# Kernel tuning notes

Measured on AMD Instinct MI355X. Metric: run time of the kernel, lower is better.

The kernel has to match this reference:

```python
import jax, jax.numpy as jnp
import numpy as np

ALPHA = 0.2  # LeakyReLU slope in GAT
OUT_SLOPE = 0.01  # default nn.LeakyyReLU slope for self.out
B, E, IN_DIM, HID, HEADS = 4, 2048, 32, 18, 3
DH = HID // HEADS  # per-head out dim = 6


def _leaky(x, slope):
    return jnp.where(x > 0, x, slope * x)


def _gat_head(x, adj, W, a):
    # x: [B,E,in], W: [in,dh], a: [2*dh,1]
    h = jnp.einsum('bei,id->bed', x, W)                      # [B,E,dh]
    d = h.shape[-1]
    # score[b,i,j] = leakyrelu(a . concat(h_i, h_j)) = leakyrelu(h_i.a1 + h_j.a2)
    e1 = jnp.einsum('bed,d->be', h, a[:d, 0])
    e2 = jnp.einsum('bed,d->be', h, a[d:, 0])
    score = _leaky(e1[:, :, None] + e2[:, None, :], ALPHA)   # [B,E,E]
    scores = jnp.where(adj == 1.0, score, 0.0)
    logits = jnp.where(adj > 0.0, scores, -30.0)
    att = jax.nn.softmax(logits, axis=2)                     # softmax over j
    # h_prime[b,j,d] = sum_i att[b,i,j] * h[b,i,d]  (torch sums over dim=1)
    h_prime = jnp.einsum('bij,bid->bjd', att, h)
    return jax.nn.elu(h_prime)  # concat=True -> elu


def _gat_multihead(x, adj, Ws, As):
    # Ws: [H,in,dh], As: [H,2*dh,1]
    outs = jax.vmap(lambda W, a: _gat_head(x, adj, W, a))(Ws, As)  # [H,B,E,dh]
    H, b, e, d = outs.shape
    return jnp.moveaxis(outs, 0, 2).reshape(b, e, H * d)  # concat heads last-dim


def _gcn(x, adj2d, W, b):
    return adj2d @ (x @ W) + b


def setup_inputs() -> dict:
    key = jax.random.key(0)
    ks = jax.random.split(key, 16)
    node_input = jax.random.normal(ks[0], (B, E, IN_DIM), jnp.float32)
    uv_filed = jax.random.normal(ks[1], (B, E, IN_DIM), jnp.float32)
    adj = jax.random.randint(ks[2], (B, E, E), 0, 2).astype(jnp.float32)
    s = 0.1
    Wt1 = jax.random.normal(ks[3], (HEADS, IN_DIM, DH), jnp.float32) * s
    at1 = jax.random.normal(ks[4], (HEADS, 2 * DH, 1), jnp.float32) * s
    Wt2 = jax.random.normal(ks[5], (HEADS, IN_DIM, DH), jnp.float32) * s
    at2 = jax.random.normal(ks[6], (HEADS, 2 * DH, 1), jnp.float32) * s
    Wg1 = jax.random.normal(ks[7], (HID, 16), jnp.float32) * s
    bg1 = jnp.zeros((16,), jnp.float32)
    Wg2 = jax.random.normal(ks[8], (16, 2), jnp.float32) * s
    bg2 = jnp.zeros((2,), jnp.float32)
    Wo1 = jax.random.normal(ks[9], (HID, 16), jnp.float32) * s
    bo1 = jnp.zeros((16,), jnp.float32)
    Wo2 = jax.random.normal(ks[10], (16, 2), jnp.float32) * s
    bo2 = jnp.zeros((2,), jnp.float32)
    return dict(node_input=node_input, uv_filed=uv_filed, adj=adj,
                Wt1=Wt1, at1=at1, Wt2=Wt2, at2=at2,
                Wg1=Wg1, bg1=bg1, Wg2=Wg2, bg2=bg2,
                Wo1=Wo1, bo1=bo1, Wo2=Wo2, bo2=bo2)


def reference(node_input, uv_filed, adj, Wt1, at1, Wt2, at2,
              Wg1, bg1, Wg2, bg2, Wo1, bo1, Wo2, bo2):
    h = _gat_multihead(node_input, adj, Wt1, at1)  # [B,E,18]
    o = _gat_multihead(uv_filed, adj, Wt2, at2)    # [B,E,18]
    a0 = adj[0]
    Y = jax.nn.relu(_gcn(h[0], a0, Wg1, bg1))
    O = jax.nn.relu(_gcn(o[0], a0, Wo1, bo1))
    Y = _gcn(Y, a0, Wg2, bg2)
    O = _gcn(O, a0, Wo2, bo2)
    return (jax.nn.log_softmax(Y, axis=1), _leaky(O, OUT_SLOPE))
```

## Files before the change

kernel.cpp:

```cpp
#include <hip/hip_runtime.h>
#include <hip/hip_bf16.h>


__global__ __launch_bounds__(256) void k1_features(
    const float* __restrict__ node, const float* __restrict__ uv,
    const float* __restrict__ Wt1, const float* __restrict__ at1,
    const float* __restrict__ Wt2, const float* __restrict__ at2,
    float* __restrict__ hcol, float* __restrict__ pack1, float* __restrict__ pack2) {
  __shared__ float sW[192];
  __shared__ float sA[12];
  int b = blockIdx.x;
  int g = b / 24;
  int h = (b / 8) % 3;
  int e = (b % 8) * 256 + threadIdx.x;
  const float* W = (g ? Wt2 : Wt1) + h * 192;
  const float* A = (g ? at2 : at1) + h * 12;
  const float* x = (g ? uv : node) + e * 32;
  if (threadIdx.x < 192) sW[threadIdx.x] = W[threadIdx.x];
  if (threadIdx.x < 12) sA[threadIdx.x] = A[threadIdx.x];
  __syncthreads();
  float xv[32];
#pragma unroll
  for (int i = 0; i < 32; ++i) xv[i] = x[i];
  float hv[6];
#pragma unroll
  for (int d = 0; d < 6; ++d) hv[d] = 0.f;
#pragma unroll
  for (int i = 0; i < 32; ++i)
#pragma unroll
    for (int d = 0; d < 6; ++d) hv[d] += xv[i] * sW[i * 6 + d];
  float e1 = 0.f, e2 = 0.f;
#pragma unroll
  for (int d = 0; d < 6; ++d) {
    e1 += hv[d] * sA[d];
    e2 += hv[d] * sA[6 + d];
  }
  int c = g * 3 + h;
#pragma unroll
  for (int d = 0; d < 6; ++d) hcol[(c * 6 + d) * 2048 + e] = hv[d];
  pack1[c * 2048 + e] = e1;
  pack1[(6 + c) * 2048 + e] = __expf(e1);
  pack1[(12 + c) * 2048 + e] = __expf(0.2f * e1);
  pack2[c * 2048 + e] = e2;
  pack2[(6 + c) * 2048 + e] = __expf(e2);
  pack2[(12 + c) * 2048 + e] = __expf(0.2f * e2);
}

__global__ __launch_bounds__(384) void k2_rowsum(
    const float* __restrict__ adj0, const float* __restrict__ pack1,
    const float* __restrict__ pack2, float* __restrict__ invrs) {
  int tid = threadIdx.x;
  int c = tid >> 6, lane = tid & 63;
  int i0 = blockIdx.x * 4;
  const float4* adj4 = (const float4*)adj0;
  const float4* p2_4 = (const float4*)pack2;
  float e1r[4], p1r[4], q1r[4], sum[4];
#pragma unroll
  for (int r = 0; r < 4; ++r) {
    e1r[r] = pack1[c * 2048 + i0 + r];
    p1r[r] = pack1[(6 + c) * 2048 + i0 + r];
    q1r[r] = pack1[(12 + c) * 2048 + i0 + r];
    sum[r] = 0.f;
  }
#pragma unroll
  for (int it = 0; it < 8; ++it) {
    int j4 = it * 64 + lane;
    float4 e2 = p2_4[c * 512 + j4];
    float4 p2 = p2_4[(6 + c) * 512 + j4];
    float4 q2 = p2_4[(12 + c) * 512 + j4];
    float4 av[4];
#pragma unroll
    for (int r = 0; r < 4; ++r) av[r] = adj4[(i0 + r) * 512 + j4];
#pragma unroll
    for (int r = 0; r < 4; ++r) {
      float s0, s1, s2, s3;
      { float e = e1r[r] + e2.x; bool p = e > 0.f;
        s0 = av[r].x * (p ? p1r[r] : q1r[r]) * (p ? p2.x : q2.x); }
      { float e = e1r[r] + e2.y; bool p = e > 0.f;
        s1 = av[r].y * (p ? p1r[r] : q1r[r]) * (p ? p2.y : q2.y); }
      { float e = e1r[r] + e2.z; bool p = e > 0.f;
        s2 = av[r].z * (p ? p1r[r] : q1r[r]) * (p ? p2.z : q2.z); }
      { float e = e1r[r] + e2.w; bool p = e > 0.f;
        s3 = av[r].w * (p ? p1r[r] : q1r[r]) * (p ? p2.w : q2.w); }
      sum[r] += (s0 + s1) + (s2 + s3);
    }
  }
#pragma unroll
  for (int r = 0; r < 4; ++r) {
#pragma unroll
    for (int off = 32; off > 0; off >>= 1) sum[r] += __shfl_down(sum[r], off);
  }
  if (lane == 0) {
#pragma unroll
    for (int r = 0; r < 4; ++r) invrs[c * 2048 + i0 + r] = 1.0f / sum[r];
  }
}

__global__ __launch_bounds__(384) void k3_hprime(
    const float* __restrict__ adj0, const float* __restrict__ hcol,
    const float* __restrict__ pack1, const float* __restrict__ pack2,
    const float* __restrict__ invrs, float* __restrict__ hp) {
  __shared__ float sAdj[64 * 64];
  __shared__ float4 sPack[6 * 64];
  __shared__ float sHS[6 * 64 * 8];
  float4* sAdj4 = (float4*)sAdj;
  const float4* adj4 = (const float4*)adj0;
  float4* sHS4 = (float4*)sHS;
  int tid = threadIdx.x;
  int c6 = tid >> 6, jl = tid & 63;
  int j0 = blockIdx.x * 64;
  int j = j0 + jl;
  float e2v = pack2[c6 * 2048 + j];
  float p2v = pack2[(6 + c6) * 2048 + j];
  float q2v = pack2[(12 + c6) * 2048 + j];
  float acc0 = 0.f, acc1 = 0.f, acc2 = 0.f, acc3 = 0.f, acc4 = 0.f, acc5 = 0.f;
  int ibeg = blockIdx.y * 128, iend = ibeg + 128;
  for (int i0 = ibeg; i0 < iend; i0 += 64) {
    __syncthreads();
    for (int idx = tid; idx < 1024; idx += 384) {
      int ii = idx >> 4, c4 = idx & 15;
      sAdj4[ii * 16 + c4] = adj4[(i0 + ii) * 512 + (j0 >> 2) + c4];
    }
    {
      int cc = c6, ii = jl;
      float e1 = pack1[cc * 2048 + i0 + ii];
      float p1 = pack1[(6 + cc) * 2048 + i0 + ii];
      float q1 = pack1[(12 + cc) * 2048 + i0 + ii];
      sPack[cc * 64 + ii] = make_float4(e1, p1, q1, 0.f);
      float iv = invrs[cc * 2048 + i0 + ii];
#pragma unroll
      for (int d = 0; d < 6; ++d)
        sHS[(cc * 64 + ii) * 8 + d] = hcol[(cc * 6 + d) * 2048 + i0 + ii] * iv;
      sHS[(cc * 64 + ii) * 8 + 6] = 0.f;
      sHS[(cc * 64 + ii) * 8 + 7] = 0.f;
    }
    __syncthreads();
#pragma unroll 8
    for (int ii = 0; ii < 64; ++ii) {
      float adjv = sAdj[ii * 64 + jl];
      float4 pk = sPack[c6 * 64 + ii];
      float4 h0 = sHS4[(c6 * 64 + ii) * 2];
      float4 h1 = sHS4[(c6 * 64 + ii) * 2 + 1];
      float e = pk.x + e2v;
      bool pos = e > 0.f;
      float w = adjv * (pos ? pk.y : pk.z) * (pos ? p2v : q2v);
      acc0 += w * h0.x;
      acc1 += w * h0.y;
      acc2 += w * h0.z;
      acc3 += w * h0.w;
      acc4 += w * h1.x;
      acc5 += w * h1.y;
    }
  }
  int kb = c6 * 6;
  atomicAdd(&hp[(kb + 0) * 2048 + j], acc0);
  atomicAdd(&hp[(kb + 1) * 2048 + j], acc1);
  atomicAdd(&hp[(kb + 2) * 2048 + j], acc2);
  atomicAdd(&hp[(kb + 3) * 2048 + j], acc3);
  atomicAdd(&hp[(kb + 4) * 2048 + j], acc4);
  atomicAdd(&hp[(kb + 5) * 2048 + j], acc5);
}

__global__ __launch_bounds__(256) void k4_T(
    const float* __restrict__ hp, const float* __restrict__ Wg1,
    const float* __restrict__ Wo1, float* __restrict__ T) {
  __shared__ float sHP[32 * 37];
  __shared__ float sWg[288], sWo[288];
  int tid = threadIdx.x;
  int j0 = blockIdx.x * 32;
  for (int idx = tid; idx < 288; idx += 256) {
    sWg[idx] = Wg1[idx];
    sWo[idx] = Wo1[idx];
  }
  for (int idx = tid; idx < 1152; idx += 256) {
    int r = idx >> 5, jl = idx & 31;
    sHP[jl * 37 + r] = hp[r * 2048 + j0 + jl];
  }
  __syncthreads();
  int jl = tid & 31, wq = tid >> 5;
  int gat = wq >> 2;
  int c0 = (wq & 3) * 4;
  const float* Wp = gat ? sWo : sWg;
  float acc[4];
#pragma unroll
  for (int t = 0; t < 4; ++t) acc[t] = 0.f;
#pragma unroll
  for (int r = 0; r < 18; ++r) {
    float x = sHP[jl * 37 + gat * 18 + r];
    float hc = x > 0.f ? x : __expf(x) - 1.f;
#pragma unroll
    for (int t = 0; t < 4; ++t) acc[t] += hc * Wp[r * 16 + c0 + t];
  }
#pragma unroll
  for (int t = 0; t < 4; ++t) T[(j0 + jl) * 32 + gat * 16 + c0 + t] = acc[t];
}

__global__ __launch_bounds__(256) void k5_gcn1(
    const float* __restrict__ adj0, const float* __restrict__ T,
    float* __restrict__ Craw) {
  int tid = threadIdx.x;
  int lane = tid & 63, w = tid >> 6;
  int c = lane & 31, rh = lane >> 5;
  int r = blockIdx.x * 8 + w * 2 + rh;
  int k0 = blockIdx.y * 512;
  const float* arow = adj0 + (size_t)r * 2048 + k0;
  const float* tcol = T + (size_t)k0 * 32 + c;
  float acc = 0.f;
#pragma unroll 16
  for (int k = 0; k < 512; ++k) {
    acc += arow[k] * tcol[k * 32];
  }
  atomicAdd(&Craw[r * 32 + c], acc);
}

__global__ __launch_bounds__(256) void k6_T2(
    const float* __restrict__ Craw, const float* __restrict__ bg1,
    const float* __restrict__ Wg2, const float* __restrict__ bo1,
    const float* __restrict__ Wo2, float* __restrict__ T2) {
  int tid = threadIdx.x;
  int wave = tid >> 6, lane = tid & 63;
  int j = blockIdx.x * 8 + wave * 2 + (lane >> 5);
  int cl = lane & 31;
  int gat = cl >> 4, cc = cl & 15;
  float x = Craw[j * 32 + cl];
  x += gat ? bo1[cc] : bg1[cc];
  x = x > 0.f ? x : 0.f;
  float wa = gat ? Wo2[cc * 2 + 0] : Wg2[cc * 2 + 0];
  float wb = gat ? Wo2[cc * 2 + 1] : Wg2[cc * 2 + 1];
  float pa = x * wa, pb = x * wb;
#pragma unroll
  for (int m = 8; m > 0; m >>= 1) {
    pa += __shfl_xor(pa, m);
    pb += __shfl_xor(pb, m);
  }
  if (cc == 0) {
    T2[j * 4 + gat * 2 + 0] = pa;
    T2[j * 4 + gat * 2 + 1] = pb;
  }
}

__global__ __launch_bounds__(256) void k7_final(
    const float* __restrict__ adj0, const float* __restrict__ T2,
    const float* __restrict__ bg2, const float* __restrict__ bo2,
    float* __restrict__ out) {
  int tid = threadIdx.x;
  int lane = tid & 63, w = tid >> 6;
  int r = blockIdx.x * 4 + w;
  const float4* adj4 = (const float4*)adj0;
  const float4* T24 = (const float4*)T2;
  float4 acc = make_float4(0.f, 0.f, 0.f, 0.f);
#pragma unroll
  for (int it = 0; it < 8; ++it) {
    int k4 = it * 64 + lane;
    float4 av = adj4[r * 512 + k4];
    float4 t0 = T24[k4 * 4 + 0];
    float4 t1 = T24[k4 * 4 + 1];
    float4 t2 = T24[k4 * 4 + 2];
    float4 t3 = T24[k4 * 4 + 3];
    acc.x += av.x * t0.x + av.y * t1.x + av.z * t2.x + av.w * t3.x;
    acc.y += av.x * t0.y + av.y * t1.y + av.z * t2.y + av.w * t3.y;
    acc.z += av.x * t0.z + av.y * t1.z + av.z * t2.z + av.w * t3.z;
    acc.w += av.x * t0.w + av.y * t1.w + av.z * t2.w + av.w * t3.w;
  }
#pragma unroll
  for (int off = 32; off > 0; off >>= 1) {
    acc.x += __shfl_down(acc.x, off);
    acc.y += __shfl_down(acc.y, off);
    acc.z += __shfl_down(acc.z, off);
    acc.w += __shfl_down(acc.w, off);
  }
  if (lane == 0) {
    float y0 = acc.x + bg2[0], y1 = acc.y + bg2[1];
    float m = fmaxf(y0, y1);
    float ls = m + logf(__expf(y0 - m) + __expf(y1 - m));
    out[r * 2 + 0] = y0 - ls;
    out[r * 2 + 1] = y1 - ls;
    float o0 = acc.z + bo2[0], o1 = acc.w + bo2[1];
    out[4096 + r * 2 + 0] = o0 > 0.f ? o0 : 0.01f * o0;
    out[4096 + r * 2 + 1] = o1 > 0.f ? o1 : 0.01f * o1;
  }
}

extern "C" void kernel_launch(void* const* d_in, const int* in_sizes, int n_in,
                              void* d_out, int out_size, void* d_ws, size_t ws_size,
                              hipStream_t stream) {
  const float* node = (const float*)d_in[0];
  const float* uv = (const float*)d_in[1];
  const float* adj = (const float*)d_in[2];
  const float* Wt1 = (const float*)d_in[3];
  const float* at1 = (const float*)d_in[4];
  const float* Wt2 = (const float*)d_in[5];
  const float* at2 = (const float*)d_in[6];
  const float* Wg1 = (const float*)d_in[7];
  const float* bg1 = (const float*)d_in[8];
  const float* Wg2 = (const float*)d_in[9];
  const float* bg2 = (const float*)d_in[10];
  const float* Wo1 = (const float*)d_in[11];
  const float* bo1 = (const float*)d_in[12];
  const float* Wo2 = (const float*)d_in[13];
  const float* bo2 = (const float*)d_in[14];
  float* ws = (float*)d_ws;
  float* hcol = ws;
  float* pack1 = ws + 73728;
  float* pack2 = ws + 110592;
  float* invrs = ws + 147456;
  float* T = ws + 159744;
  float* T2 = ws + 225280;
  float* hp = ws + 233472;
  float* Craw = ws + 307200;
  float* out = (float*)d_out;

  hipMemsetAsync(hp, 0, (73728 + 65536) * sizeof(float), stream);
  k1_features<<<48, 256, 0, stream>>>(node, uv, Wt1, at1, Wt2, at2, hcol, pack1, pack2);
  k2_rowsum<<<512, 384, 0, stream>>>(adj, pack1, pack2, invrs);
  k3_hprime<<<dim3(32, 16), 384, 0, stream>>>(adj, hcol, pack1, pack2, invrs, hp);
  k4_T<<<64, 256, 0, stream>>>(hp, Wg1, Wo1, T);
  k5_gcn1<<<dim3(256, 4), 256, 0, stream>>>(adj, T, Craw);
  k6_T2<<<256, 256, 0, stream>>>(Craw, bg1, Wg2, bo1, Wo2, T2);
  k7_final<<<512, 256, 0, stream>>>(adj, T2, bg2, bo2, out);
}
```

Baseline: 196.6 us.

## Compress adjacency into a bitmask once and read it in all adj-consuming kernels

A new first kernel packs the 2048x2048 float adjacency row into 32-bit ballot masks. The rowsum, h-prime aggregation, and both GCN matmul kernels then read bits instead of the 16MB float matrix. The h-prime and GCN-1 kernels are also retiled: h-prime gets 128-column tiles with two accumulator sets per thread and no inner i-loop, and GCN-1 stages the mask and T tiles in shared memory. This cuts repeated global reads of adj, at the cost of an extra launch. It assumes adjacency entries are exactly 0 or 1.

```diff
diff --git a/kernel.cpp b/kernel.cpp
--- a/kernel.cpp
+++ b/kernel.cpp
@@ -1,6 +1,20 @@
 #include <hip/hip_runtime.h>
 #include <hip/hip_bf16.h>
 
+
+__global__ __launch_bounds__(256) void k0_bitmask(
+    const float* __restrict__ adj0, unsigned int* __restrict__ bm) {
+  int lane = threadIdx.x & 63, w = threadIdx.x >> 6;
+  int row = blockIdx.x * 4 + w;
+  const float* arow = adj0 + (size_t)row * 2048;
+#pragma unroll 4
+  for (int it = 0; it < 32; ++it) {
+    float v = arow[it * 64 + lane];
+    unsigned long long mask = __ballot(v == 1.0f);
+    if (lane == 0) bm[row * 64 + it * 2] = (unsigned int)mask;
+    else if (lane == 32) bm[row * 64 + it * 2 + 1] = (unsigned int)(mask >> 32);
+  }
+}
 
 __global__ __launch_bounds__(256) void k1_features(
     const float* __restrict__ node, const float* __restrict__ uv,
@@ -47,118 +61,129 @@
 }
 
 __global__ __launch_bounds__(384) void k2_rowsum(
-    const float* __restrict__ adj0, const float* __restrict__ pack1,
+    const unsigned int* __restrict__ bm, const float* __restrict__ pack1,
     const float* __restrict__ pack2, float* __restrict__ invrs) {
   int tid = threadIdx.x;
   int c = tid >> 6, lane = tid & 63;
-  int i0 = blockIdx.x * 4;
-  const float4* adj4 = (const float4*)adj0;
+  int i0 = blockIdx.x * 8;
   const float4* p2_4 = (const float4*)pack2;
-  float e1r[4], p1r[4], q1r[4], sum[4];
-#pragma unroll
-  for (int r = 0; r < 4; ++r) {
+  float e1r[8], p1r[8], q1r[8], sum[8];
+#pragma unroll
+  for (int r = 0; r < 8; ++r) {
     e1r[r] = pack1[c * 2048 + i0 + r];
     p1r[r] = pack1[(6 + c) * 2048 + i0 + r];
     q1r[r] = pack1[(12 + c) * 2048 + i0 + r];
     sum[r] = 0.f;
   }
+  int sh = (lane & 7) * 4;
 #pragma unroll
   for (int it = 0; it < 8; ++it) {
     int j4 = it * 64 + lane;
     float4 e2 = p2_4[c * 512 + j4];
     float4 p2 = p2_4[(6 + c) * 512 + j4];
     float4 q2 = p2_4[(12 + c) * 512 + j4];
-    float4 av[4];
-#pragma unroll
-    for (int r = 0; r < 4; ++r) av[r] = adj4[(i0 + r) * 512 + j4];
-#pragma unroll
-    for (int r = 0; r < 4; ++r) {
-      float s0, s1, s2, s3;
+    int wbase = it * 8 + (lane >> 3);
+    float abx, aby, abz, abw;
+#pragma unroll
+    for (int r = 0; r < 8; ++r) {
+      unsigned int wd = bm[(i0 + r) * 64 + wbase] >> sh;
       { float e = e1r[r] + e2.x; bool p = e > 0.f;
-        s0 = av[r].x * (p ? p1r[r] : q1r[r]) * (p ? p2.x : q2.x); }
+        abx = (p ? p1r[r] : q1r[r]) * (p ? p2.x : q2.x); }
       { float e = e1r[r] + e2.y; bool p = e > 0.f;
-        s1 = av[r].y * (p ? p1r[r] : q1r[r]) * (p ? p2.y : q2.y); }
+        aby = (p ? p1r[r] : q1r[r]) * (p ? p2.y : q2.y); }
       { float e = e1r[r] + e2.z; bool p = e > 0.f;
-        s2 = av[r].z * (p ? p1r[r] : q1r[r]) * (p ? p2.z : q2.z); }
+        abz = (p ? p1r[r] : q1r[r]) * (p ? p2.z : q2.z); }
       { float e = e1r[r] + e2.w; bool p = e > 0.f;
-        s3 = av[r].w * (p ? p1r[r] : q1r[r]) * (p ? p2.w : q2.w); }
-      sum[r] += (s0 + s1) + (s2 + s3);
+        abw = (p ? p1r[r] : q1r[r]) * (p ? p2.w : q2.w); }
+      float s = ((wd & 1u) ? abx : 0.f) + ((wd & 2u) ? aby : 0.f) +
+                ((wd & 4u) ? abz : 0.f) + ((wd & 8u) ? abw : 0.f);
+      sum[r] += s;
     }
   }
 #pragma unroll
-  for (int r = 0; r < 4; ++r) {
+  for (int r = 0; r < 8; ++r) {
 #pragma unroll
     for (int off = 32; off > 0; off >>= 1) sum[r] += __shfl_down(sum[r], off);
   }
   if (lane == 0) {
 #pragma unroll
-    for (int r = 0; r < 4; ++r) invrs[c * 2048 + i0 + r] = 1.0f / sum[r];
+    for (int r = 0; r < 8; ++r) invrs[c * 2048 + i0 + r] = 1.0f / sum[r];
   }
 }
 
 __global__ __launch_bounds__(384) void k3_hprime(
-    const float* __restrict__ adj0, const float* __restrict__ hcol,
+    const unsigned int* __restrict__ bm, const float* __restrict__ hcol,
     const float* __restrict__ pack1, const float* __restrict__ pack2,
     const float* __restrict__ invrs, float* __restrict__ hp) {
-  __shared__ float sAdj[64 * 64];
   __shared__ float4 sPack[6 * 64];
   __shared__ float sHS[6 * 64 * 8];
-  float4* sAdj4 = (float4*)sAdj;
-  const float4* adj4 = (const float4*)adj0;
+  __shared__ unsigned int sM[64 * 4];
   float4* sHS4 = (float4*)sHS;
   int tid = threadIdx.x;
   int c6 = tid >> 6, jl = tid & 63;
-  int j0 = blockIdx.x * 64;
-  int j = j0 + jl;
-  float e2v = pack2[c6 * 2048 + j];
-  float p2v = pack2[(6 + c6) * 2048 + j];
-  float q2v = pack2[(12 + c6) * 2048 + j];
-  float acc0 = 0.f, acc1 = 0.f, acc2 = 0.f, acc3 = 0.f, acc4 = 0.f, acc5 = 0.f;
-  int ibeg = blockIdx.y * 128, iend = ibeg + 128;
-  for (int i0 = ibeg; i0 < iend; i0 += 64) {
-    __syncthreads();
-    for (int idx = tid; idx < 1024; idx += 384) {
-      int ii = idx >> 4, c4 = idx & 15;
-      sAdj4[ii * 16 + c4] = adj4[(i0 + ii) * 512 + (j0 >> 2) + c4];
+  int j0 = blockIdx.x * 128;
+  int i0 = blockIdx.y * 64;
+  int jA = j0 + jl, jB = jA + 64;
+  float e2A = pack2[c6 * 2048 + jA];
+  float p2A = pack2[(6 + c6) * 2048 + jA];
+  float q2A = pack2[(12 + c6) * 2048 + jA];
+  float e2B = pack2[c6 * 2048 + jB];
+  float p2B = pack2[(6 + c6) * 2048 + jB];
+  float q2B = pack2[(12 + c6) * 2048 + jB];
+  {
+    int cc = c6, ii = jl;
+    float e1 = pack1[cc * 2048 + i0 + ii];
+    float p1 = pack1[(6 + cc) * 2048 + i0 + ii];
+    float q1 = pack1[(12 + cc) * 2048 + i0 + ii];
+    sPack[cc * 64 + ii] = make_float4(e1, p1, q1, 0.f);
+    float iv = invrs[cc * 2048 + i0 + ii];
+#pragma unroll
+    for (int d = 0; d < 6; ++d)
+      sHS[(cc * 64 + ii) * 8 + d] = hcol[(cc * 6 + d) * 2048 + i0 + ii] * iv;
+    sHS[(cc * 64 + ii) * 8 + 6] = 0.f;
+    sHS[(cc * 64 + ii) * 8 + 7] = 0.f;
+  }
+  if (tid < 256) sM[tid] = bm[(size_t)(i0 + (tid >> 2)) * 64 + (j0 >> 5) + (tid & 3)];
+  __syncthreads();
+  float aA0 = 0.f, aA1 = 0.f, aA2 = 0.f, aA3 = 0.f, aA4 = 0.f, aA5 = 0.f;
+  float aB0 = 0.f, aB1 = 0.f, aB2 = 0.f, aB3 = 0.f, aB4 = 0.f, aB5 = 0.f;
+  int hi = jl >> 5;
+  int shj = jl & 31;
+#pragma unroll 8
+  for (int ii = 0; ii < 64; ++ii) {
+    float4 pk = sPack[c6 * 64 + ii];
+    float4 h0 = sHS4[(c6 * 64 + ii) * 2];
+    float4 h1 = sHS4[(c6 * 64 + ii) * 2 + 1];
+    unsigned int wdA = sM[ii * 4 + hi];
+    unsigned int wdB = sM[ii * 4 + 2 + hi];
+    {
+      float e = pk.x + e2A; bool p = e > 0.f;
+      float ab = (p ? pk.y : pk.z) * (p ? p2A : q2A);
+      float wgt = ((wdA >> shj) & 1u) ? ab : 0.f;
+      aA0 += wgt * h0.x; aA1 += wgt * h0.y; aA2 += wgt * h0.z;
+      aA3 += wgt * h0.w; aA4 += wgt * h1.x; aA5 += wgt * h1.y;
     }
     {
-      int cc = c6, ii = jl;
-      float e1 = pack1[cc * 2048 + i0 + ii];
-      float p1 = pack1[(6 + cc) * 2048 + i0 + ii];
-      float q1 = pack1[(12 + cc) * 2048 + i0 + ii];
-      sPack[cc * 64 + ii] = make_float4(e1, p1, q1, 0.f);
-      float iv = invrs[cc * 2048 + i0 + ii];
-#pragma unroll
-      for (int d = 0; d < 6; ++d)
-        sHS[(cc * 64 + ii) * 8 + d] = hcol[(cc * 6 + d) * 2048 + i0 + ii] * iv;
-      sHS[(cc * 64 + ii) * 8 + 6] = 0.f;
-      sHS[(cc * 64 + ii) * 8 + 7] = 0.f;
+      float e = pk.x + e2B; bool p = e > 0.f;
+      float ab = (p ? pk.y : pk.z) * (p ? p2B : q2B);
+      float wgt = ((wdB >> shj) & 1u) ? ab : 0.f;
+      aB0 += wgt * h0.x; aB1 += wgt * h0.y; aB2 += wgt * h0.z;
+      aB3 += wgt * h0.w; aB4 += wgt * h1.x; aB5 += wgt * h1.y;
     }
-    __syncthreads();
-#pragma unroll 8
-    for (int ii = 0; ii < 64; ++ii) {
-      float adjv = sAdj[ii * 64 + jl];
-      float4 pk = sPack[c6 * 64 + ii];
-      float4 h0 = sHS4[(c6 * 64 + ii) * 2];
-      float4 h1 = sHS4[(c6 * 64 + ii) * 2 + 1];
-      float e = pk.x + e2v;
-      bool pos = e > 0.f;
-      float w = adjv * (pos ? pk.y : pk.z) * (pos ? p2v : q2v);
-      acc0 += w * h0.x;
-      acc1 += w * h0.y;
-      acc2 += w * h0.z;
-      acc3 += w * h0.w;
-      acc4 += w * h1.x;
-      acc5 += w * h1.y;
-    }
   }
   int kb = c6 * 6;
-  atomicAdd(&hp[(kb + 0) * 2048 + j], acc0);
-  atomicAdd(&hp[(kb + 1) * 2048 + j], acc1);
-  atomicAdd(&hp[(kb + 2) * 2048 + j], acc2);
-  atomicAdd(&hp[(kb + 3) * 2048 + j], acc3);
-  atomicAdd(&hp[(kb + 4) * 2048 + j], acc4);
-  atomicAdd(&hp[(kb + 5) * 2048 + j], acc5);
+  atomicAdd(&hp[(kb + 0) * 2048 + jA], aA0);
+  atomicAdd(&hp[(kb + 1) * 2048 + jA], aA1);
+  atomicAdd(&hp[(kb + 2) * 2048 + jA], aA2);
+  atomicAdd(&hp[(kb + 3) * 2048 + jA], aA3);
+  atomicAdd(&hp[(kb + 4) * 2048 + jA], aA4);
+  atomicAdd(&hp[(kb + 5) * 2048 + jA], aA5);
+  atomicAdd(&hp[(kb + 0) * 2048 + jB], aB0);
+  atomicAdd(&hp[(kb + 1) * 2048 + jB], aB1);
+  atomicAdd(&hp[(kb + 2) * 2048 + jB], aB2);
+  atomicAdd(&hp[(kb + 3) * 2048 + jB], aB3);
+  atomicAdd(&hp[(kb + 4) * 2048 + jB], aB4);
+  atomicAdd(&hp[(kb + 5) * 2048 + jB], aB5);
 }
 
 __global__ __launch_bounds__(256) void k4_T(
@@ -196,21 +221,39 @@
 }
 
 __global__ __launch_bounds__(256) void k5_gcn1(
-    const float* __restrict__ adj0, const float* __restrict__ T,
+    const unsigned int* __restrict__ bm, const float* __restrict__ T,
     float* __restrict__ Craw) {
-  int tid = threadIdx.x;
-  int lane = tid & 63, w = tid >> 6;
-  int c = lane & 31, rh = lane >> 5;
-  int r = blockIdx.x * 8 + w * 2 + rh;
-  int k0 = blockIdx.y * 512;
-  const float* arow = adj0 + (size_t)r * 2048 + k0;
-  const float* tcol = T + (size_t)k0 * 32 + c;
-  float acc = 0.f;
+  __shared__ unsigned int sM[64 * 4];
+  __shared__ float4 sT4[128 * 8];
+  const float4* T4 = (const float4*)T;
+  int tid = threadIdx.x;
+  int rl = tid & 31, cg = tid >> 5;
+  int i0 = blockIdx.x * 64;
+  int k0 = blockIdx.y * 128;
+  if (tid < 256) sM[tid] = bm[(size_t)(i0 + (tid >> 2)) * 64 + (k0 >> 5) + (tid & 3)];
+  for (int idx = tid; idx < 1024; idx += 256) sT4[idx] = T4[k0 * 8 + idx];
+  __syncthreads();
+  float a0x = 0.f, a0y = 0.f, a0z = 0.f, a0w = 0.f;
+  float a1x = 0.f, a1y = 0.f, a1z = 0.f, a1w = 0.f;
+#pragma unroll
+  for (int wi = 0; wi < 4; ++wi) {
+    unsigned int wA = sM[rl * 4 + wi];
+    unsigned int wB = sM[(rl + 32) * 4 + wi];
 #pragma unroll 16
-  for (int k = 0; k < 512; ++k) {
-    acc += arow[k] * tcol[k * 32];
-  }
-  atomicAdd(&Craw[r * 32 + c], acc);
+    for (int kb = 0; kb < 32; ++kb) {
+      float4 t = sT4[(wi * 32 + kb) * 8 + cg];
+      float mA = (float)((wA >> kb) & 1u);
+      float mB = (float)((wB >> kb) & 1u);
+      a0x += mA * t.x; a0y += mA * t.y; a0z += mA * t.z; a0w += mA * t.w;
+      a1x += mB * t.x; a1y += mB * t.y; a1z += mB * t.z; a1w += mB * t.w;
+    }
+  }
+  float* d0 = &Craw[(i0 + rl) * 32 + cg * 4];
+  atomicAdd(d0 + 0, a0x); atomicAdd(d0 + 1, a0y);
+  atomicAdd(d0 + 2, a0z); atomicAdd(d0 + 3, a0w);
+  float* d1 = &Craw[(i0 + rl + 32) * 32 + cg * 4];
+  atomicAdd(d1 + 0, a1x); atomicAdd(d1 + 1, a1y);
+  atomicAdd(d1 + 2, a1z); atomicAdd(d1 + 3, a1w);
 }
 
 __global__ __launch_bounds__(256) void k6_T2(
@@ -240,27 +283,25 @@
 }
 
 __global__ __launch_bounds__(256) void k7_final(
-    const float* __restrict__ adj0, const float* __restrict__ T2,
+    const unsigned int* __restrict__ bm, const float* __restrict__ T2,
     const float* __restrict__ bg2, const float* __restrict__ bo2,
     float* __restrict__ out) {
   int tid = threadIdx.x;
   int lane = tid & 63, w = tid >> 6;
   int r = blockIdx.x * 4 + w;
-  const float4* adj4 = (const float4*)adj0;
   const float4* T24 = (const float4*)T2;
   float4 acc = make_float4(0.f, 0.f, 0.f, 0.f);
-#pragma unroll
-  for (int it = 0; it < 8; ++it) {
-    int k4 = it * 64 + lane;
-    float4 av = adj4[r * 512 + k4];
-    float4 t0 = T24[k4 * 4 + 0];
-    float4 t1 = T24[k4 * 4 + 1];
-    float4 t2 = T24[k4 * 4 + 2];
-    float4 t3 = T24[k4 * 4 + 3];
-    acc.x += av.x * t0.x + av.y * t1.x + av.z * t2.x + av.w * t3.x;
-    acc.y += av.x * t0.y + av.y * t1.y + av.z * t2.y + av.w * t3.y;
-    acc.z += av.x * t0.z + av.y * t1.z + av.z * t2.z + av.w * t3.z;
-    acc.w += av.x * t0.w + av.y * t1.w + av.z * t2.w + av.w * t3.w;
+  int sh = lane & 31;
+#pragma unroll 8
+  for (int it = 0; it < 32; ++it) {
+    int k = it * 64 + lane;
+    unsigned int wd = bm[r * 64 + it * 2 + (lane >> 5)];
+    float m = (float)((wd >> sh) & 1u);
+    float4 t = T24[k];
+    acc.x += m * t.x;
+    acc.y += m * t.y;
+    acc.z += m * t.z;
+    acc.w += m * t.w;
   }
 #pragma unroll
   for (int off = 32; off > 0; off >>= 1) {
@@ -308,14 +349,16 @@
   float* T2 = ws + 225280;
   float* hp = ws + 233472;
   float* Craw = ws + 307200;
+  unsigned int* bm = (unsigned int*)(ws + 372736);
   float* out = (float*)d_out;
 
   hipMemsetAsync(hp, 0, (73728 + 65536) * sizeof(float), stream);
+  k0_bitmask<<<512, 256, 0, stream>>>(adj, bm);
   k1_features<<<48, 256, 0, stream>>>(node, uv, Wt1, at1, Wt2, at2, hcol, pack1, pack2);
-  k2_rowsum<<<512, 384, 0, stream>>>(adj, pack1, pack2, invrs);
-  k3_hprime<<<dim3(32, 16), 384, 0, stream>>>(adj, hcol, pack1, pack2, invrs, hp);
+  k2_rowsum<<<256, 384, 0, stream>>>(bm, pack1, pack2, invrs);
+  k3_hprime<<<dim3(16, 32), 384, 0, stream>>>(bm, hcol, pack1, pack2, invrs, hp);
   k4_T<<<64, 256, 0, stream>>>(hp, Wg1, Wo1, T);
-  k5_gcn1<<<dim3(256, 4), 256, 0, stream>>>(adj, T, Craw);
+  k5_gcn1<<<dim3(32, 16), 256, 0, stream>>>(bm, T, Craw);
   k6_T2<<<256, 256, 0, stream>>>(Craw, bg1, Wg2, bo1, Wo2, T2);
-  k7_final<<<512, 256, 0, stream>>>(adj, T2, bg2, bo2, out);
-}
+  k7_final<<<512, 256, 0, stream>>>(bm, T2, bg2, bo2, out);
+}
```

After: 212.2 us. 1.08x slower.
